# Optimization experiments

Hardware: AMD Instinct MI355X
Metric: run time of the kernel (lower is better)

Reference implementation:

```python
import jax, jax.numpy as jnp
from jax import lax
import numpy as np

DIM, RESO, HEADS, SPLIT, B = 128, 112, 4, 7, 2
HID = 4 * DIM  # mlp_ratio=4


def _ln(x, g, b):
    m = x.mean(-1, keepdims=True)
    v = ((x - m) ** 2).mean(-1, keepdims=True)
    return (x - m) * lax.rsqrt(v + 1e-5) * g + b


def _lepe_attn(q, k, v, cw, cb, H, W, H_sp, W_sp, nh):
    # q,k,v: [B, H*W, C] (C = branch dim); cw: depthwise conv weight [C,1,3,3]
    Bq, L, C = q.shape
    hd = C // nh
    scale = hd ** -0.5
    nHw, nWw = H // H_sp, W // W_sp

    def to_win(t):  # [B,H,W,C] -> [B*nHw*nWw, nh, H_sp*W_sp, hd]
        t = t.reshape(Bq, nHw, H_sp, nWw, W_sp, C).transpose(0, 1, 3, 2, 4, 5)
        return t.reshape(-1, H_sp * W_sp, nh, hd).transpose(0, 2, 1, 3)

    qw = to_win(q.reshape(Bq, H, W, C)) * scale
    kw = to_win(k.reshape(Bq, H, W, C))

    # v path: window partition in NCHW, depthwise conv LePE per window
    vimg = v.transpose(0, 2, 1).reshape(Bq, C, H, W)
    vimg = vimg.reshape(Bq, C, nHw, H_sp, nWw, W_sp).transpose(0, 2, 4, 1, 3, 5)
    vimg = vimg.reshape(-1, C, H_sp, W_sp)  # [B', C, H_sp, W_sp]
    lepe = lax.conv_general_dilated(vimg, cw, (1, 1), 'SAME', feature_group_count=C,
                                    dimension_numbers=('NCHW', 'OIHW', 'NCHW'))
    lepe = lepe + cb[None, :, None, None]
    vw = vimg.reshape(-1, nh, hd, H_sp * W_sp).transpose(0, 1, 3, 2)
    lepe = lepe.reshape(-1, nh, hd, H_sp * W_sp).transpose(0, 1, 3, 2)

    attn = jax.nn.softmax(jnp.einsum('whnd,whmd->whnm', qw, kw), axis=-1)
    o = jnp.einsum('whnm,whmd->whnd', attn, vw) + lepe  # [B', nh, S, hd]

    # windows2img
    o = o.transpose(0, 2, 1, 3).reshape(-1, H_sp * W_sp, C)
    o = o.reshape(Bq, nHw, nWw, H_sp, W_sp, C).transpose(0, 1, 3, 2, 4, 5)
    return o.reshape(Bq, H * W, C)


def setup_inputs() -> dict:
    key = jax.random.key(0)
    ks = jax.random.split(key, 16)
    s = 0.02
    Cb = DIM // 2
    return {
        'x': jax.random.normal(ks[0], (B, RESO * RESO, DIM), jnp.float32),
        'g1': jnp.ones((DIM,), jnp.float32),
        'b1': jnp.zeros((DIM,), jnp.float32),
        'w_qkv': s * jax.random.normal(ks[1], (3 * DIM, DIM), jnp.float32),
        'conv_w0': s * jax.random.normal(ks[2], (Cb, 1, 3, 3), jnp.float32),
        'conv_b0': jnp.zeros((Cb,), jnp.float32),
        'conv_w1': s * jax.random.normal(ks[3], (Cb, 1, 3, 3), jnp.float32),
        'conv_b1': jnp.zeros((Cb,), jnp.float32),
        'w_proj': s * jax.random.normal(ks[4], (DIM, DIM), jnp.float32),
        'b_proj': jnp.zeros((DIM,), jnp.float32),
        'g2': jnp.ones((DIM,), jnp.float32),
        'b2': jnp.zeros((DIM,), jnp.float32),
        'w_fc1': s * jax.random.normal(ks[5], (HID, DIM), jnp.float32),
        'b_fc1': jnp.zeros((HID,), jnp.float32),
        'w_fc2': s * jax.random.normal(ks[6], (DIM, HID), jnp.float32),
        'b_fc2': jnp.zeros((DIM,), jnp.float32),
    }


def reference(x, g1, b1, w_qkv, conv_w0, conv_b0, conv_w1, conv_b1,
              w_proj, b_proj, g2, b2, w_fc1, b_fc1, w_fc2, b_fc2):
    Bq, L, C = x.shape
    Cb = C // 2
    nh_b = HEADS // 2
    img = _ln(x, g1, b1)
    qkv = (img @ w_qkv.T).reshape(Bq, L, 3, C)  # qkv_bias=False
    q, k, v = qkv[:, :, 0], qkv[:, :, 1], qkv[:, :, 2]
    # branch 0: horizontal stripes (H_sp=RESO, W_sp=SPLIT) on first half of channels
    x1 = _lepe_attn(q[..., :Cb], k[..., :Cb], v[..., :Cb], conv_w0, conv_b0,
                    RESO, RESO, RESO, SPLIT, nh_b)
    # branch 1: vertical stripes (H_sp=SPLIT, W_sp=RESO) on second half
    x2 = _lepe_attn(q[..., Cb:], k[..., Cb:], v[..., Cb:], conv_w1, conv_b1,
                    RESO, RESO, SPLIT, RESO, nh_b)
    att = jnp.concatenate([x1, x2], axis=2)
    att = att @ w_proj.T + b_proj
    x = x + att  # drop_path = identity (prob 0)
    y = _ln(x, g2, b2)
    h = jax.nn.gelu(y @ w_fc1.T + b_fc1, approximate=False)
    x = x + (h @ w_fc2.T + b_fc2)
    return x
```

## Files before the change

### kernel.cpp

```cpp
#include <hip/hip_runtime.h>
#include <cstdint>

#define LTOK 12544
#define BATCH 2
#define CDIM 128
#define C3 384
#define RES 112
#define NROWS (BATCH * LTOK)
#define CHUNKS 784
#define GRID 256
#define SCALE 0.17677669529663687f

typedef __attribute__((ext_vector_type(8))) short bf16x8;
typedef __attribute__((ext_vector_type(4))) float f32x4;

__device__ inline ushort f2b(float f) {
    union { float f; unsigned u; } v; v.f = f;
    unsigned r = (v.u + 0x7FFFu + ((v.u >> 16) & 1u)) >> 16;
    return (ushort)r;
}
__device__ inline float b2f(ushort u) {
    union { float f; unsigned u; } v; v.u = ((unsigned)u) << 16; return v.f;
}
__device__ inline float gelu_f(float a) {
    float u2 = 1.5957691216f * (a + 0.044715f * a * a * a);
    return a - a / (__expf(u2) + 1.0f);
}

__device__ inline void nij(int n, int branch, int& i, int& j) {
    if (branch == 0) { i = n / 7; j = n - i * 7; }
    else             { i = n / 112; j = n - i * 112; }
}

__global__ __launch_bounds__(256) void k_cvt(const float* __restrict__ w0, const float* __restrict__ w1,
        const float* __restrict__ w2, const float* __restrict__ w3,
        ushort* __restrict__ o0, ushort* __restrict__ o1,
        ushort* __restrict__ o2, ushort* __restrict__ o3)
{
    int idx = blockIdx.x * 256 + threadIdx.x;
    const float* src; ushort* dst; int vi;
    if      (idx < 12288) { src = w0; dst = o0; vi = idx; }
    else if (idx < 16384) { src = w1; dst = o1; vi = idx - 12288; }
    else if (idx < 32768) { src = w2; dst = o2; vi = idx - 16384; }
    else                  { src = w3; dst = o3; vi = idx - 32768; }
    float4 v = ((const float4*)src)[vi];
    ushort4 r; r.x = f2b(v.x); r.y = f2b(v.y); r.z = f2b(v.z); r.w = f2b(v.w);
    ((ushort4*)dst)[vi] = r;
}

__global__ __launch_bounds__(512) void k_ln_qkv(const float* __restrict__ x,
        const float* __restrict__ g1, const float* __restrict__ b1,
        const ushort* __restrict__ wqkv_bf, ushort* __restrict__ qkv)
{
    __shared__ ushort ys[32 * 136];
    const int tid = threadIdx.x;
    const int wv = tid >> 6, lane = tid & 63;
    const int c16 = lane & 15, g = lane >> 4;

    bf16x8 wr[3][4];
    #pragma unroll
    for (int t = 0; t < 3; ++t)
        #pragma unroll
        for (int kc = 0; kc < 4; ++kc)
            wr[t][kc] = *(const bf16x8*)&wqkv_bf[(wv * 48 + t * 16 + c16) * CDIM + kc * 32 + g * 8];

    const int r = tid >> 4, l16 = tid & 15;
    float4 gv0 = *(const float4*)(g1 + l16 * 8);
    float4 gv4 = *(const float4*)(g1 + l16 * 8 + 4);
    float4 bv0 = *(const float4*)(b1 + l16 * 8);
    float4 bv4 = *(const float4*)(b1 + l16 * 8 + 4);

    for (int c = blockIdx.x; c < CHUNKS; c += GRID) {
        const long long row0 = (long long)c * 32;

        {
            const float* xr = x + (row0 + r) * CDIM + l16 * 8;
            float4 a0 = *(const float4*)xr;
            float4 a1 = *(const float4*)(xr + 4);
            float s  = a0.x + a0.y + a0.z + a0.w + a1.x + a1.y + a1.z + a1.w;
            float s2 = a0.x*a0.x + a0.y*a0.y + a0.z*a0.z + a0.w*a0.w
                     + a1.x*a1.x + a1.y*a1.y + a1.z*a1.z + a1.w*a1.w;
            #pragma unroll
            for (int m = 8; m >= 1; m >>= 1) { s += __shfl_xor(s, m, 16); s2 += __shfl_xor(s2, m, 16); }
            const float mean = s * (1.f / 128.f);
            const float var = s2 * (1.f / 128.f) - mean * mean;
            const float rs = rsqrtf(var + 1e-5f);
            ushort4 w0, w1;
            w0.x = f2b((a0.x - mean) * rs * gv0.x + bv0.x);
            w0.y = f2b((a0.y - mean) * rs * gv0.y + bv0.y);
            w0.z = f2b((a0.z - mean) * rs * gv0.z + bv0.z);
            w0.w = f2b((a0.w - mean) * rs * gv0.w + bv0.w);
            w1.x = f2b((a1.x - mean) * rs * gv4.x + bv4.x);
            w1.y = f2b((a1.y - mean) * rs * gv4.y + bv4.y);
            w1.z = f2b((a1.z - mean) * rs * gv4.z + bv4.z);
            w1.w = f2b((a1.w - mean) * rs * gv4.w + bv4.w);
            *(ushort4*)&ys[r * 136 + l16 * 8]     = w0;
            *(ushort4*)&ys[r * 136 + l16 * 8 + 4] = w1;
        }
        __syncthreads();

        bf16x8 yb[2][4];
        #pragma unroll
        for (int mt = 0; mt < 2; ++mt)
            #pragma unroll
            for (int kc = 0; kc < 4; ++kc)
                yb[mt][kc] = *(const bf16x8*)&ys[(mt * 16 + c16) * 136 + kc * 32 + g * 8];
        __syncthreads();

        #pragma unroll
        for (int t = 0; t < 3; ++t) {
            const int n0 = wv * 48 + t * 16;
            #pragma unroll
            for (int mt = 0; mt < 2; ++mt) {
                f32x4 acc = {0.f, 0.f, 0.f, 0.f};
                #pragma unroll
                for (int kc = 0; kc < 4; ++kc)
                    acc = __builtin_amdgcn_mfma_f32_16x16x32_bf16(wr[t][kc], yb[mt][kc], acc, 0, 0, 0);
                ushort4 sv;
                sv.x = f2b(acc[0]); sv.y = f2b(acc[1]); sv.z = f2b(acc[2]); sv.w = f2b(acc[3]);
                *(ushort4*)&qkv[(row0 + mt * 16 + c16) * C3 + n0 + g * 4] = sv;
            }
        }
    }
}

__global__ __launch_bounds__(256) void k_attn_mfma(const ushort* __restrict__ qkv,
        const float* __restrict__ cw0, const float* __restrict__ cb0,
        const float* __restrict__ cw1, const float* __restrict__ cb1,
        ushort* __restrict__ att)
{
    __shared__ __align__(16) ushort ks[112 * 40];
    __shared__ __align__(16) ushort vt[32 * 136];
    __shared__ __align__(16) ushort pl[4][16 * 40];
    __shared__ __align__(16) float  ol[4][16 * 36];

    const int tid = threadIdx.x;
    const int wv = tid >> 6, lane = tid & 63;
    const int g = lane >> 4, c16 = lane & 15;

    const int wh = blockIdx.x;
    const int branch = wh >> 6;
    const int idx = wh & 63;
    const int win = idx >> 1, head = idx & 1;
    const int b = win >> 4, w = win & 15;
    const int rowBase = branch ? w * 7 : 0;
    const int colBase = branch ? 0 : w * 7;
    const float* cw = branch ? cw1 : cw0;
    const float* cb = branch ? cb1 : cb0;
    const int cbase = branch * 64 + head * 32;
    const long long qkvB = (long long)b * LTOK * C3;

    {
        const int row = tid >> 3, cwd = tid & 7;
        *(unsigned*)&vt[row * 136 + 112 + cwd * 2] = 0u;
    }

    const int t0 = blockIdx.y * 7 + 2 * wv;
    const int nt = (2 * wv + 1 < 7) ? 2 : 1;

    bf16x8 qf[2];
    #pragma unroll
    for (int t = 0; t < 2; ++t) if (t < nt) {
        int n = (t0 + t) * 16 + c16;
        int i, j; nij(n, branch, i, j);
        const ushort* qp = qkv + qkvB + (long long)((rowBase + i) * RES + colBase + j) * C3 + cbase + g * 8;
        bf16x8 qq = *(const bf16x8*)qp;
        #pragma unroll
        for (int e = 0; e < 8; ++e) qq[e] = (short)f2b(b2f((ushort)qq[e]) * SCALE);
        qf[t] = qq;
    }

    f32x4 O00 = {0.f,0.f,0.f,0.f}, O01 = {0.f,0.f,0.f,0.f};
    f32x4 O10 = {0.f,0.f,0.f,0.f}, O11 = {0.f,0.f,0.f,0.f};
    float lsum0[4] = {0.f,0.f,0.f,0.f};
    float lsum1[4] = {0.f,0.f,0.f,0.f};

    for (int cc = 0; cc < 7; ++cc) {
        __syncthreads();
        for (int u = tid; u < 448; u += 256) {
            const int key = u >> 2, d8 = (u & 3) * 8;
            const int n = cc * 112 + key;
            int i, j; nij(n, branch, i, j);
            const ushort* base = qkv + qkvB + (long long)((rowBase + i) * RES + colBase + j) * C3 + cbase + d8;
            bf16x8 kk = *(const bf16x8*)(base + 128);
            bf16x8 vv = *(const bf16x8*)(base + 256);
            *(bf16x8*)&ks[key * 40 + d8] = kk;
            #pragma unroll
            for (int e = 0; e < 8; ++e) vt[(d8 + e) * 136 + key] = (ushort)vv[e];
        }
        __syncthreads();

        #pragma unroll
        for (int p = 0; p < 4; ++p) {
            bf16x8 kf0 = *(const bf16x8*)&ks[(p * 32 + c16) * 40 + g * 8];
            bf16x8 kf1;
            if (p < 3) kf1 = *(const bf16x8*)&ks[(p * 32 + 16 + c16) * 40 + g * 8];
            bf16x8 vf0 = *(const bf16x8*)&vt[c16 * 136 + p * 32 + g * 8];
            bf16x8 vf1 = *(const bf16x8*)&vt[(16 + c16) * 136 + p * 32 + g * 8];
            ushort* pb = &pl[wv][0];

            #pragma unroll
            for (int t = 0; t < 2; ++t) if (t < nt) {
                const bf16x8 qq = t ? qf[1] : qf[0];
                f32x4 z = {0.f,0.f,0.f,0.f};
                f32x4 S0 = __builtin_amdgcn_mfma_f32_16x16x32_bf16(qq, kf0, z, 0, 0, 0);
                f32x4 S1 = z;
                if (p < 3) S1 = __builtin_amdgcn_mfma_f32_16x16x32_bf16(qq, kf1, z, 0, 0, 0);
                ushort pw0[4], pw1[4];
                #pragma unroll
                for (int r = 0; r < 4; ++r) {
                    float e0 = __expf(S0[r]);
                    if (t) lsum1[r] += e0; else lsum0[r] += e0;
                    pw0[r] = f2b(e0);
                    if (p < 3) {
                        float e1 = __expf(S1[r]);
                        if (t) lsum1[r] += e1; else lsum0[r] += e1;
                        pw1[r] = f2b(e1);
                    } else pw1[r] = 0;
                }
                #pragma unroll
                for (int r = 0; r < 4; ++r) {
                    pb[(g * 4 + r) * 40 + c16]      = pw0[r];
                    pb[(g * 4 + r) * 40 + 16 + c16] = pw1[r];
                }
                bf16x8 pf = *(const bf16x8*)&pb[c16 * 40 + g * 8];
                if (t) {
                    O10 = __builtin_amdgcn_mfma_f32_16x16x32_bf16(pf, vf0, O10, 0, 0, 0);
                    O11 = __builtin_amdgcn_mfma_f32_16x16x32_bf16(pf, vf1, O11, 0, 0, 0);
                } else {
                    O00 = __builtin_amdgcn_mfma_f32_16x16x32_bf16(pf, vf0, O00, 0, 0, 0);
                    O01 = __builtin_amdgcn_mfma_f32_16x16x32_bf16(pf, vf1, O01, 0, 0, 0);
                }
            }
        }
    }

    const int H_sp = branch ? 7 : RES;
    const int W_sp = branch ? RES : 7;
    #pragma unroll
    for (int t = 0; t < 2; ++t) if (t < nt) {
        float* ob = &ol[wv][0];
        #pragma unroll
        for (int r = 0; r < 4; ++r) {
            float s = t ? lsum1[r] : lsum0[r];
            s += __shfl_xor(s, 1); s += __shfl_xor(s, 2);
            s += __shfl_xor(s, 4); s += __shfl_xor(s, 8);
            const float inv = 1.f / s;
            const f32x4 Oa = t ? O10 : O00;
            const f32x4 Ob = t ? O11 : O01;
            ob[(g * 4 + r) * 36 + c16]      = Oa[r] * inv;
            ob[(g * 4 + r) * 36 + 16 + c16] = Ob[r] * inv;
        }
        const int r2 = lane >> 2, db = (lane & 3) * 8;
        const int n0 = (t0 + t) * 16 + r2;
        int i0, j0; nij(n0, branch, i0, j0);
        float acc[8];
        #pragma unroll
        for (int e = 0; e < 8; ++e) acc[e] = ob[r2 * 36 + db + e] + cb[head * 32 + db + e];
        #pragma unroll
        for (int dij = 0; dij < 9; ++dij) {
            const int di = dij / 3 - 1, dj = dij % 3 - 1;
            const int ii = i0 + di, jj = j0 + dj;
            if (ii >= 0 && ii < H_sp && jj >= 0 && jj < W_sp) {
                const ushort* vp = qkv + qkvB + (long long)((rowBase + ii) * RES + colBase + jj) * C3 + 256 + cbase + db;
                bf16x8 vv = *(const bf16x8*)vp;
                #pragma unroll
                for (int e = 0; e < 8; ++e)
                    acc[e] += cw[(head * 32 + db + e) * 9 + dij] * b2f((ushort)vv[e]);
            }
        }
        const long long Lq = (long long)(rowBase + i0) * RES + colBase + j0;
        ushort* op = att + ((long long)b * LTOK + Lq) * CDIM + cbase + db;
        bf16x8 ov;
        #pragma unroll
        for (int e = 0; e < 8; ++e) ov[e] = (short)f2b(acc[e]);
        *(bf16x8*)op = ov;
    }
}

__global__ __launch_bounds__(512) void k_pmlp(const ushort* __restrict__ att,
        const ushort* __restrict__ wproj_bf, const float* __restrict__ bproj,
        const float* __restrict__ x,
        const float* __restrict__ g2, const float* __restrict__ b2,
        const ushort* __restrict__ w1bf, const float* __restrict__ bfc1,
        const ushort* __restrict__ w2bf, const float* __restrict__ bfc2,
        float* __restrict__ out)
{
    __shared__ float  xs[32 * 132];
    __shared__ ushort ys[32 * 136];
    __shared__ ushort hs[32 * 520];
    const int tid = threadIdx.x;
    const int wv = tid >> 6, lane = tid & 63;
    const int c16 = lane & 15, g = lane >> 4;

    bf16x8 wpr[4];
    #pragma unroll
    for (int kc = 0; kc < 4; ++kc)
        wpr[kc] = *(const bf16x8*)&wproj_bf[(wv * 16 + c16) * CDIM + kc * 32 + g * 8];
    bf16x8 w1r[4][4];
    #pragma unroll
    for (int t = 0; t < 4; ++t)
        #pragma unroll
        for (int kc = 0; kc < 4; ++kc)
            w1r[t][kc] = *(const bf16x8*)&w1bf[(wv * 64 + t * 16 + c16) * CDIM + kc * 32 + g * 8];
    const float4 bpv = *(const float4*)&bproj[wv * 16 + g * 4];
    float4 b1v[4];
    #pragma unroll
    for (int t = 0; t < 4; ++t) b1v[t] = *(const float4*)&bfc1[wv * 64 + t * 16 + g * 4];
    const float4 b2v = *(const float4*)&bfc2[wv * 16 + g * 4];

    const int r = tid >> 4, l16 = tid & 15;
    float4 gv0 = *(const float4*)(g2 + l16 * 8);
    float4 gv4 = *(const float4*)(g2 + l16 * 8 + 4);
    float4 bv0 = *(const float4*)(b2 + l16 * 8);
    float4 bv4 = *(const float4*)(b2 + l16 * 8 + 4);

    for (int c = blockIdx.x; c < CHUNKS; c += GRID) {
        const long long row0 = (long long)c * 32;

        f32x4 resid[2];
        {
            bf16x8 ab[2][4];
            #pragma unroll
            for (int mt = 0; mt < 2; ++mt)
                #pragma unroll
                for (int kc = 0; kc < 4; ++kc)
                    ab[mt][kc] = *(const bf16x8*)&att[(row0 + mt * 16 + c16) * CDIM + kc * 32 + g * 8];
            const int col = wv * 16 + g * 4;
            #pragma unroll
            for (int mt = 0; mt < 2; ++mt) {
                f32x4 a = {0.f, 0.f, 0.f, 0.f};
                #pragma unroll
                for (int kc = 0; kc < 4; ++kc)
                    a = __builtin_amdgcn_mfma_f32_16x16x32_bf16(wpr[kc], ab[mt][kc], a, 0, 0, 0);
                float4 xv = *(const float4*)&x[(row0 + mt * 16 + c16) * CDIM + col];
                f32x4 rr;
                rr[0] = a[0] + xv.x + bpv.x;
                rr[1] = a[1] + xv.y + bpv.y;
                rr[2] = a[2] + xv.z + bpv.z;
                rr[3] = a[3] + xv.w + bpv.w;
                resid[mt] = rr;
                *(float4*)&xs[(mt * 16 + c16) * 132 + col] = make_float4(rr[0], rr[1], rr[2], rr[3]);
            }
        }
        __syncthreads();

        {
            float4 a0 = *(const float4*)&xs[r * 132 + l16 * 8];
            float4 a1 = *(const float4*)&xs[r * 132 + l16 * 8 + 4];
            float s  = a0.x + a0.y + a0.z + a0.w + a1.x + a1.y + a1.z + a1.w;
            float s2 = a0.x*a0.x + a0.y*a0.y + a0.z*a0.z + a0.w*a0.w
                     + a1.x*a1.x + a1.y*a1.y + a1.z*a1.z + a1.w*a1.w;
            #pragma unroll
            for (int m = 8; m >= 1; m >>= 1) { s += __shfl_xor(s, m, 16); s2 += __shfl_xor(s2, m, 16); }
            const float mean = s * (1.f / 128.f);
            const float var = s2 * (1.f / 128.f) - mean * mean;
            const float rs = rsqrtf(var + 1e-5f);
            ushort4 w0, w1;
            w0.x = f2b((a0.x - mean) * rs * gv0.x + bv0.x);
            w0.y = f2b((a0.y - mean) * rs * gv0.y + bv0.y);
            w0.z = f2b((a0.z - mean) * rs * gv0.z + bv0.z);
            w0.w = f2b((a0.w - mean) * rs * gv0.w + bv0.w);
            w1.x = f2b((a1.x - mean) * rs * gv4.x + bv4.x);
            w1.y = f2b((a1.y - mean) * rs * gv4.y + bv4.y);
            w1.z = f2b((a1.z - mean) * rs * gv4.z + bv4.z);
            w1.w = f2b((a1.w - mean) * rs * gv4.w + bv4.w);
            *(ushort4*)&ys[r * 136 + l16 * 8]     = w0;
            *(ushort4*)&ys[r * 136 + l16 * 8 + 4] = w1;
        }
        __syncthreads();

        bf16x8 yb[2][4];
        #pragma unroll
        for (int mt = 0; mt < 2; ++mt)
            #pragma unroll
            for (int kc = 0; kc < 4; ++kc)
                yb[mt][kc] = *(const bf16x8*)&ys[(mt * 16 + c16) * 136 + kc * 32 + g * 8];

        #pragma unroll
        for (int t = 0; t < 4; ++t) {
            #pragma unroll
            for (int mt = 0; mt < 2; ++mt) {
                f32x4 a = {0.f, 0.f, 0.f, 0.f};
                #pragma unroll
                for (int kc = 0; kc < 4; ++kc)
                    a = __builtin_amdgcn_mfma_f32_16x16x32_bf16(w1r[t][kc], yb[mt][kc], a, 0, 0, 0);
                ushort4 sv;
                sv.x = f2b(gelu_f(a[0] + b1v[t].x));
                sv.y = f2b(gelu_f(a[1] + b1v[t].y));
                sv.z = f2b(gelu_f(a[2] + b1v[t].z));
                sv.w = f2b(gelu_f(a[3] + b1v[t].w));
                *(ushort4*)&hs[(mt * 16 + c16) * 520 + wv * 64 + t * 16 + g * 4] = sv;
            }
        }

        bf16x8 w2r[16];
        #pragma unroll
        for (int kc = 0; kc < 16; ++kc)
            w2r[kc] = *(const bf16x8*)&w2bf[(wv * 16 + c16) * 512 + kc * 32 + g * 8];

        __syncthreads();

        f32x4 acc2[2] = {{0.f,0.f,0.f,0.f},{0.f,0.f,0.f,0.f}};
        #pragma unroll
        for (int kc = 0; kc < 16; ++kc) {
            bf16x8 hb[2];
            #pragma unroll
            for (int mt = 0; mt < 2; ++mt)
                hb[mt] = *(const bf16x8*)&hs[(mt * 16 + c16) * 520 + kc * 32 + g * 8];
            #pragma unroll
            for (int mt = 0; mt < 2; ++mt)
                acc2[mt] = __builtin_amdgcn_mfma_f32_16x16x32_bf16(w2r[kc], hb[mt], acc2[mt], 0, 0, 0);
        }

        {
            const int col = wv * 16 + g * 4;
            #pragma unroll
            for (int mt = 0; mt < 2; ++mt) {
                const long long row = row0 + mt * 16 + c16;
                float4 o;
                o.x = acc2[mt][0] + resid[mt][0] + b2v.x;
                o.y = acc2[mt][1] + resid[mt][1] + b2v.y;
                o.z = acc2[mt][2] + resid[mt][2] + b2v.z;
                o.w = acc2[mt][3] + resid[mt][3] + b2v.w;
                *(float4*)&out[row * CDIM + col] = o;
            }
        }
    }
}

extern "C" void kernel_launch(void* const* d_in, const int* in_sizes, int n_in,
                              void* d_out, int out_size, void* d_ws, size_t ws_size,
                              hipStream_t stream) {
    const float* x     = (const float*)d_in[0];
    const float* g1    = (const float*)d_in[1];
    const float* b1    = (const float*)d_in[2];
    const float* wqkv  = (const float*)d_in[3];
    const float* cw0   = (const float*)d_in[4];
    const float* cb0   = (const float*)d_in[5];
    const float* cw1   = (const float*)d_in[6];
    const float* cb1   = (const float*)d_in[7];
    const float* wproj = (const float*)d_in[8];
    const float* bproj = (const float*)d_in[9];
    const float* g2    = (const float*)d_in[10];
    const float* b2    = (const float*)d_in[11];
    const float* wfc1  = (const float*)d_in[12];
    const float* bfc1  = (const float*)d_in[13];
    const float* wfc2  = (const float*)d_in[14];
    const float* bfc2  = (const float*)d_in[15];

    char* wsb = (char*)d_ws;
    ushort* qkv_bf   = (ushort*)wsb;
    ushort* att_bf   = (ushort*)(wsb + 19267584);
    char*   wbase    = wsb + 19267584 + 6422528;
    ushort* wqkv_bf  = (ushort*)(wbase);
    ushort* wproj_bf = (ushort*)(wbase + 98304);
    ushort* wfc1_bf  = (ushort*)(wbase + 98304 + 32768);
    ushort* wfc2_bf  = (ushort*)(wbase + 98304 + 32768 + 131072);

    float* out = (float*)d_out;

    k_cvt<<<192, 256, 0, stream>>>(wqkv, wproj, wfc1, wfc2, wqkv_bf, wproj_bf, wfc1_bf, wfc2_bf);
    k_ln_qkv<<<GRID, 512, 0, stream>>>(x, g1, b1, wqkv_bf, qkv_bf);
    k_attn_mfma<<<dim3(128, 7), 256, 0, stream>>>(qkv_bf, cw0, cb0, cw1, cb1, att_bf);
    k_pmlp<<<GRID, 512, 0, stream>>>(att_bf, wproj_bf, bproj, x, g2, b2,
                                     wfc1_bf, bfc1, wfc2_bf, bfc2, out);
}
```

Measured before the change: 109.9 us.

## Stage whole window K/V in shared memory once per block, fewer larger blocks

The attention kernel now loads all 784 keys and values of a window-head into dynamic shared memory (about 140KB) in a single pass, instead of reloading 112-key chunks for each of seven query-tile blocks. The grid shrinks from 128x7 blocks of 256 threads to 128x2 blocks of 512 threads, and each wave loops over query tiles against the full key set. This cuts redundant global K/V traffic and the per-chunk barriers. In exchange only 256 blocks run, each with large LDS, which limits occupancy to one block per CU and can leave the GPU underfilled.

```diff
diff --git a/kernel.cpp b/kernel.cpp
--- a/kernel.cpp
+++ b/kernel.cpp
@@ -10,6 +10,14 @@
 #define CHUNKS 784
 #define GRID 256
 #define SCALE 0.17677669529663687f
+
+#define KS_STRIDE 40
+#define VT_STRIDE 800
+#define KS_USHORTS (784 * KS_STRIDE)
+#define VT_USHORTS (32 * VT_STRIDE)
+#define PL_USHORTS (8 * 16 * 40)
+#define OL_FLOATS  (8 * 16 * 36)
+#define ATTN_SMEM  (2 * (KS_USHORTS + VT_USHORTS + PL_USHORTS) + 4 * OL_FLOATS)
 
 typedef __attribute__((ext_vector_type(8))) short bf16x8;
 typedef __attribute__((ext_vector_type(4))) float f32x4;
@@ -124,15 +132,16 @@
     }
 }
 
-__global__ __launch_bounds__(256) void k_attn_mfma(const ushort* __restrict__ qkv,
+__global__ __launch_bounds__(512) void k_attn2(const ushort* __restrict__ qkv,
         const float* __restrict__ cw0, const float* __restrict__ cb0,
         const float* __restrict__ cw1, const float* __restrict__ cb1,
         ushort* __restrict__ att)
 {
-    __shared__ __align__(16) ushort ks[112 * 40];
-    __shared__ __align__(16) ushort vt[32 * 136];
-    __shared__ __align__(16) ushort pl[4][16 * 40];
-    __shared__ __align__(16) float  ol[4][16 * 36];
+    extern __shared__ __align__(16) char smem[];
+    ushort* ks = (ushort*)smem;
+    ushort* vt = ks + KS_USHORTS;
+    ushort* pl = vt + VT_USHORTS;
+    float*  ol = (float*)(pl + PL_USHORTS);
 
     const int tid = threadIdx.x;
     const int wv = tid >> 6, lane = tid & 63;
@@ -150,109 +159,101 @@
     const int cbase = branch * 64 + head * 32;
     const long long qkvB = (long long)b * LTOK * C3;
 
-    {
-        const int row = tid >> 3, cwd = tid & 7;
-        *(unsigned*)&vt[row * 136 + 112 + cwd * 2] = 0u;
-    }
-
-    const int t0 = blockIdx.y * 7 + 2 * wv;
-    const int nt = (2 * wv + 1 < 7) ? 2 : 1;
-
-    bf16x8 qf[2];
-    #pragma unroll
-    for (int t = 0; t < 2; ++t) if (t < nt) {
-        int n = (t0 + t) * 16 + c16;
-        int i, j; nij(n, branch, i, j);
-        const ushort* qp = qkv + qkvB + (long long)((rowBase + i) * RES + colBase + j) * C3 + cbase + g * 8;
-        bf16x8 qq = *(const bf16x8*)qp;
-        #pragma unroll
-        for (int e = 0; e < 8; ++e) qq[e] = (short)f2b(b2f((ushort)qq[e]) * SCALE);
-        qf[t] = qq;
-    }
-
-    f32x4 O00 = {0.f,0.f,0.f,0.f}, O01 = {0.f,0.f,0.f,0.f};
-    f32x4 O10 = {0.f,0.f,0.f,0.f}, O11 = {0.f,0.f,0.f,0.f};
-    float lsum0[4] = {0.f,0.f,0.f,0.f};
-    float lsum1[4] = {0.f,0.f,0.f,0.f};
-
-    for (int cc = 0; cc < 7; ++cc) {
-        __syncthreads();
-        for (int u = tid; u < 448; u += 256) {
-            const int key = u >> 2, d8 = (u & 3) * 8;
-            const int n = cc * 112 + key;
-            int i, j; nij(n, branch, i, j);
-            const ushort* base = qkv + qkvB + (long long)((rowBase + i) * RES + colBase + j) * C3 + cbase + d8;
-            bf16x8 kk = *(const bf16x8*)(base + 128);
-            bf16x8 vv = *(const bf16x8*)(base + 256);
-            *(bf16x8*)&ks[key * 40 + d8] = kk;
-            #pragma unroll
-            for (int e = 0; e < 8; ++e) vt[(d8 + e) * 136 + key] = (ushort)vv[e];
-        }
-        __syncthreads();
-
-        #pragma unroll
-        for (int p = 0; p < 4; ++p) {
-            bf16x8 kf0 = *(const bf16x8*)&ks[(p * 32 + c16) * 40 + g * 8];
-            bf16x8 kf1;
-            if (p < 3) kf1 = *(const bf16x8*)&ks[(p * 32 + 16 + c16) * 40 + g * 8];
-            bf16x8 vf0 = *(const bf16x8*)&vt[c16 * 136 + p * 32 + g * 8];
-            bf16x8 vf1 = *(const bf16x8*)&vt[(16 + c16) * 136 + p * 32 + g * 8];
-            ushort* pb = &pl[wv][0];
-
-            #pragma unroll
-            for (int t = 0; t < 2; ++t) if (t < nt) {
-                const bf16x8 qq = t ? qf[1] : qf[0];
-                f32x4 z = {0.f,0.f,0.f,0.f};
-                f32x4 S0 = __builtin_amdgcn_mfma_f32_16x16x32_bf16(qq, kf0, z, 0, 0, 0);
-                f32x4 S1 = z;
-                if (p < 3) S1 = __builtin_amdgcn_mfma_f32_16x16x32_bf16(qq, kf1, z, 0, 0, 0);
-                ushort pw0[4], pw1[4];
-                #pragma unroll
-                for (int r = 0; r < 4; ++r) {
-                    float e0 = __expf(S0[r]);
-                    if (t) lsum1[r] += e0; else lsum0[r] += e0;
-                    pw0[r] = f2b(e0);
-                    if (p < 3) {
-                        float e1 = __expf(S1[r]);
-                        if (t) lsum1[r] += e1; else lsum0[r] += e1;
-                        pw1[r] = f2b(e1);
-                    } else pw1[r] = 0;
-                }
-                #pragma unroll
-                for (int r = 0; r < 4; ++r) {
-                    pb[(g * 4 + r) * 40 + c16]      = pw0[r];
-                    pb[(g * 4 + r) * 40 + 16 + c16] = pw1[r];
-                }
-                bf16x8 pf = *(const bf16x8*)&pb[c16 * 40 + g * 8];
-                if (t) {
-                    O10 = __builtin_amdgcn_mfma_f32_16x16x32_bf16(pf, vf0, O10, 0, 0, 0);
-                    O11 = __builtin_amdgcn_mfma_f32_16x16x32_bf16(pf, vf1, O11, 0, 0, 0);
-                } else {
-                    O00 = __builtin_amdgcn_mfma_f32_16x16x32_bf16(pf, vf0, O00, 0, 0, 0);
-                    O01 = __builtin_amdgcn_mfma_f32_16x16x32_bf16(pf, vf1, O01, 0, 0, 0);
-                }
-            }
-        }
-    }
-
+    if (tid < 256) {
+        const int row = tid >> 3, c2 = (tid & 7) * 2;
+        *(unsigned*)&vt[row * VT_STRIDE + 784 + c2] = 0u;
+    }
+
+    for (int u = tid; u < 1568; u += 512) {
+        const int kp = u >> 2, d8 = (u & 3) * 8;
+        const int n0 = 2 * kp;
+        int i, j; nij(n0, branch, i, j);
+        const long long L0 = (long long)(rowBase + i) * RES + colBase + j;
+        long long L1;
+        if (branch) L1 = L0 + 1;
+        else        L1 = (j == 6) ? (L0 + RES - 6) : (L0 + 1);
+        const ushort* p0 = qkv + qkvB + L0 * C3 + cbase + d8;
+        const ushort* p1 = qkv + qkvB + L1 * C3 + cbase + d8;
+        bf16x8 k0 = *(const bf16x8*)(p0 + 128);
+        bf16x8 k1 = *(const bf16x8*)(p1 + 128);
+        bf16x8 v0 = *(const bf16x8*)(p0 + 256);
+        bf16x8 v1 = *(const bf16x8*)(p1 + 256);
+        *(bf16x8*)&ks[(n0)     * KS_STRIDE + d8] = k0;
+        *(bf16x8*)&ks[(n0 + 1) * KS_STRIDE + d8] = k1;
+        #pragma unroll
+        for (int e = 0; e < 8; ++e) {
+            ushort2 pr; pr.x = (ushort)v0[e]; pr.y = (ushort)v1[e];
+            *(ushort2*)&vt[(d8 + e) * VT_STRIDE + n0] = pr;
+        }
+    }
+    __syncthreads();
+
+    const int tbase = blockIdx.y ? 25 : 0;
+    const int ntile = blockIdx.y ? 24 : 25;
     const int H_sp = branch ? 7 : RES;
     const int W_sp = branch ? RES : 7;
-    #pragma unroll
-    for (int t = 0; t < 2; ++t) if (t < nt) {
-        float* ob = &ol[wv][0];
+    ushort* pb = pl + wv * (16 * 40);
+    float*  ob = ol + wv * (16 * 36);
+
+    for (int t = wv; t < ntile; t += 8) {
+        const int gt = tbase + t;
+        bf16x8 qq;
+        {
+            int n = gt * 16 + c16;
+            int i, j; nij(n, branch, i, j);
+            const ushort* qp = qkv + qkvB + (long long)((rowBase + i) * RES + colBase + j) * C3 + cbase + g * 8;
+            qq = *(const bf16x8*)qp;
+            #pragma unroll
+            for (int e = 0; e < 8; ++e) qq[e] = (short)f2b(b2f((ushort)qq[e]) * SCALE);
+        }
+
+        f32x4 O0 = {0.f,0.f,0.f,0.f}, O1 = {0.f,0.f,0.f,0.f};
+        float lsum[4] = {0.f,0.f,0.f,0.f};
+
+        for (int p = 0; p < 25; ++p) {
+            bf16x8 kf0 = *(const bf16x8*)&ks[(p * 32 + c16) * KS_STRIDE + g * 8];
+            bf16x8 vf0 = *(const bf16x8*)&vt[c16 * VT_STRIDE + p * 32 + g * 8];
+            bf16x8 vf1 = *(const bf16x8*)&vt[(16 + c16) * VT_STRIDE + p * 32 + g * 8];
+            f32x4 z = {0.f,0.f,0.f,0.f};
+            f32x4 S0 = __builtin_amdgcn_mfma_f32_16x16x32_bf16(qq, kf0, z, 0, 0, 0);
+            f32x4 S1 = z;
+            if (p < 24) {
+                bf16x8 kf1 = *(const bf16x8*)&ks[(p * 32 + 16 + c16) * KS_STRIDE + g * 8];
+                S1 = __builtin_amdgcn_mfma_f32_16x16x32_bf16(qq, kf1, z, 0, 0, 0);
+            }
+            ushort pw0[4], pw1[4];
+            #pragma unroll
+            for (int r = 0; r < 4; ++r) {
+                float e0 = __expf(S0[r]);
+                lsum[r] += e0;
+                pw0[r] = f2b(e0);
+                if (p < 24) {
+                    float e1 = __expf(S1[r]);
+                    lsum[r] += e1;
+                    pw1[r] = f2b(e1);
+                } else pw1[r] = 0;
+            }
+            #pragma unroll
+            for (int r = 0; r < 4; ++r) {
+                pb[(g * 4 + r) * 40 + c16]      = pw0[r];
+                pb[(g * 4 + r) * 40 + 16 + c16] = pw1[r];
+            }
+            bf16x8 pf = *(const bf16x8*)&pb[c16 * 40 + g * 8];
+            O0 = __builtin_amdgcn_mfma_f32_16x16x32_bf16(pf, vf0, O0, 0, 0, 0);
+            O1 = __builtin_amdgcn_mfma_f32_16x16x32_bf16(pf, vf1, O1, 0, 0, 0);
+        }
+
         #pragma unroll
         for (int r = 0; r < 4; ++r) {
-            float s = t ? lsum1[r] : lsum0[r];
+            float s = lsum[r];
             s += __shfl_xor(s, 1); s += __shfl_xor(s, 2);
             s += __shfl_xor(s, 4); s += __shfl_xor(s, 8);
             const float inv = 1.f / s;
-            const f32x4 Oa = t ? O10 : O00;
-            const f32x4 Ob = t ? O11 : O01;
-            ob[(g * 4 + r) * 36 + c16]      = Oa[r] * inv;
-            ob[(g * 4 + r) * 36 + 16 + c16] = Ob[r] * inv;
+            ob[(g * 4 + r) * 36 + c16]      = O0[r] * inv;
+            ob[(g * 4 + r) * 36 + 16 + c16] = O1[r] * inv;
         }
         const int r2 = lane >> 2, db = (lane & 3) * 8;
-        const int n0 = (t0 + t) * 16 + r2;
+        const int n0 = gt * 16 + r2;
         int i0, j0; nij(n0, branch, i0, j0);
         float acc[8];
         #pragma unroll
@@ -460,9 +461,16 @@
 
     float* out = (float*)d_out;
 
+    static bool attr_set = false;
+    if (!attr_set) {
+        hipFuncSetAttribute((const void*)k_attn2,
+                            hipFuncAttributeMaxDynamicSharedMemorySize, ATTN_SMEM);
+        attr_set = true;
+    }
+
     k_cvt<<<192, 256, 0, stream>>>(wqkv, wproj, wfc1, wfc2, wqkv_bf, wproj_bf, wfc1_bf, wfc2_bf);
     k_ln_qkv<<<GRID, 512, 0, stream>>>(x, g1, b1, wqkv_bf, qkv_bf);
-    k_attn_mfma<<<dim3(128, 7), 256, 0, stream>>>(qkv_bf, cw0, cb0, cw1, cb1, att_bf);
+    k_attn2<<<dim3(128, 2), 512, ATTN_SMEM, stream>>>(qkv_bf, cw0, cb0, cw1, cb1, att_bf);
     k_pmlp<<<GRID, 512, 0, stream>>>(att_bf, wproj_bf, bproj, x, g2, b2,
                                      wfc1_bf, bfc1, wfc2_bf, bfc2, out);
 }
```

Result: no change. 111.2 us (+1.1%).
